# Optimization experiments

Measured on AMD Instinct MI355X. Metric: run time of the kernel, lower is better.

The kernel has to match this reference:

```python
import jax, jax.numpy as jnp
import numpy as np

H = 4  # attention heads


def _lstm(x, Wih, Whh, b, reverse=False):
    # x: [N, L, din] -> hidden sequence [N, L, dh]; PyTorch gate order i,f,g,o
    if reverse:
        x = x[:, ::-1, :]
    xT = jnp.swapaxes(x, 0, 1)  # [L, N, din]
    dh = Whh.shape[1]
    N = x.shape[0]

    def step(carry, xt):
        h, c = carry
        z = xt @ Wih.T + h @ Whh.T + b
        i, f, g, o = jnp.split(z, 4, axis=-1)
        c = jax.nn.sigmoid(f) * c + jax.nn.sigmoid(i) * jnp.tanh(g)
        h = jax.nn.sigmoid(o) * jnp.tanh(c)
        return (h, c), h

    h0 = jnp.zeros((N, dh), x.dtype)
    _, hs = jax.lax.scan(step, (h0, h0), xT)
    hs = jnp.swapaxes(hs, 0, 1)
    if reverse:
        hs = hs[:, ::-1, :]
    return hs


def setup_inputs() -> dict:
    key = jax.random.key(0)
    ks = jax.random.split(key, 24)
    B, T, D = 8, 128, 512
    C, L, U, V, E = 1000, 8, 16, 5000, 256

    def w(k, shape, fan_in):
        return jax.random.normal(k, shape, jnp.float32) * (1.0 / np.sqrt(fan_in))

    inp = {
        'model_embed': jax.random.normal(ks[0], (B, T, D), jnp.float32),
        'emb_table': w(ks[1], (V, E), E),
        'ctx_Wih_f': w(ks[2], (4 * E, E), E),
        'ctx_Whh_f': w(ks[3], (4 * E, E), E),
        'ctx_b_f': jnp.zeros((4 * E,), jnp.float32),
        'ctx_Wih_b': w(ks[4], (4 * E, E), E),
        'ctx_Whh_b': w(ks[5], (4 * E, E), E),
        'ctx_b_b': jnp.zeros((4 * E,), jnp.float32),
        'ctx_out_W': w(ks[6], (D, 2 * E), 2 * E),
        'hist_Wih': w(ks[7], (4 * D, D), D),
        'hist_Whh': w(ks[8], (4 * D, D), D),
        'hist_b': jnp.zeros((4 * D,), jnp.float32),
        'hist_out_W': w(ks[9], (D, D), D),
        'Wq': w(ks[10], (D, D), D),
        'Wk': w(ks[11], (D, D), D),
        'Wv': w(ks[12], (D, D), D),
        'Wo': w(ks[13], (D, D), D),
        'acoustic_W': w(ks[14], (D, D), D),
        'context_idxs': jax.random.randint(ks[15], (C, L), 0, V),
        'context_history_idx': jax.random.randint(ks[16], (B, U), 0, C),
        'context_ilens': jax.random.randint(ks[17], (C,), 1, L + 1),
        'context_history_ilens': jax.random.randint(ks[18], (B,), 1, U + 1),
    }
    return inp


def reference(model_embed, emb_table, ctx_Wih_f, ctx_Whh_f, ctx_b_f,
              ctx_Wih_b, ctx_Whh_b, ctx_b_b, ctx_out_W,
              hist_Wih, hist_Whh, hist_b, hist_out_W,
              Wq, Wk, Wv, Wo, acoustic_W,
              context_idxs, context_history_idx, context_ilens,
              context_history_ilens):
    C, L = context_idxs.shape
    B, T, D = model_embed.shape
    U = context_history_idx.shape[1]

    # --- ContextEncoderBiLSTM: embed -> BiLSTM -> proj -> length-masked mean ---
    emb = emb_table[context_idxs]                               # [C, L, E]
    hf = _lstm(emb, ctx_Wih_f, ctx_Whh_f, ctx_b_f)
    hb = _lstm(emb, ctx_Wih_b, ctx_Whh_b, ctx_b_b, reverse=True)
    seq = jnp.concatenate([hf, hb], -1) @ ctx_out_W.T           # [C, L, D]
    m = (jnp.arange(L)[None, :] < context_ilens[:, None]).astype(seq.dtype)
    ctx_mean = (seq * m[..., None]).sum(1) / context_ilens[:, None].astype(seq.dtype)  # [C, D]

    # --- history gather + ContextHistoryEncoderLSTM ---
    hist_in = ctx_mean[context_history_idx.reshape(-1)].reshape(B, U, D)
    hist = _lstm(hist_in, hist_Wih, hist_Whh, hist_b) @ hist_out_W.T  # [B, U, D]

    # --- fuse acoustic + history, attention-based adapter ---
    mp = model_embed @ acoustic_W.T                             # [B, T, D]
    fused = (mp[:, :, None, :] + hist[:, None, :, :]).reshape(B, T * U, D)
    dh = D // H
    q = (fused @ Wq.T).reshape(B, T * U, H, dh)
    k = (ctx_mean @ Wk.T).reshape(C, H, dh)
    v = (ctx_mean @ Wv.T).reshape(C, H, dh)
    scores = jnp.einsum('bqhd,chd->bhqc', q, k) / jnp.sqrt(jnp.asarray(dh, q.dtype))
    attn = jax.nn.softmax(scores, axis=-1)                      # [B, H, TU, C]
    out = (jnp.einsum('bhqc,chd->bqhd', attn, v).reshape(B, T * U, D) @ Wo.T)
    out = out.reshape(B, T, U, D)
    prob = attn.reshape(B, H, T, U, C).mean(1)                  # [B, T, U, C]
    logit = scores.reshape(B, H, T, U, C).mean(1)

    # --- batch greedy monotonic decoding (scan over T, full length) ---
    probT = jnp.moveaxis(prob, 1, 0)                            # [T, B, U, C]
    outT = jnp.moveaxis(out, 1, 0)                              # [T, B, U, D]
    b_idx = jnp.arange(B)

    def step(u, inp):
        p_t, o_t = inp
        u_c = jnp.minimum(u, U - 1)
        valid_u = jnp.minimum(u + 1, U - 1)
        tok = context_history_idx[b_idx, valid_u]
        blank_p = p_t[b_idx, u_c, 0]
        tok_p = p_t[b_idx, u_c, tok]
        upd = (tok_p > blank_p).astype(jnp.int32)
        return u_c + upd, (u_c, o_t[b_idx, u_c])

    u0 = jnp.zeros((B,), jnp.int32)
    _, (idx, o) = jax.lax.scan(step, u0, (probT, outT))
    o = jnp.moveaxis(o, 0, 1)                                   # [B, T, D]
    return o, logit, prob
```

## Files before the change

kernel.cpp:

```cpp
#include <hip/hip_runtime.h>
#include <math.h>

namespace {
constexpr int B_ = 8, T_ = 128, D_ = 512, C_ = 1000, L_ = 8, U_ = 16, E_ = 256, H_ = 4;
constexpr int VOC_ = 5000;
constexpr int DH_ = D_ / H_;
constexpr int E4_ = 4 * E_;
constexpr int D4_ = 4 * D_;
constexpr int TU_ = T_ * U_;
constexpr int HC_ = H_ * C_;
constexpr float SCALE_ = 0.088388347648318447f;

constexpr size_t XZ_    = 0;
constexpr size_t SM_    = 0;
constexpr size_t SH_    = SM_ + (size_t)B_ * T_ * HC_;
constexpr size_t AOUT_  = SH_ + (size_t)B_ * U_ * HC_;
constexpr size_t PVP_   = AOUT_ + (size_t)B_ * T_ * D_;
constexpr size_t REG_A  = 2ul * VOC_ * E4_;
constexpr size_t HPING  = REG_A;
constexpr size_t CST    = HPING + 2ul * C_ * E_;
constexpr size_t HPONG  = CST + 2ul * C_ * E_;
constexpr size_t HFALL  = HPONG + 2ul * C_ * E_;
constexpr size_t HBALL  = HFALL + (size_t)C_ * L_ * E_;
constexpr size_t CATM   = HBALL + (size_t)C_ * L_ * E_;
constexpr size_t CTXM   = CATM + (size_t)C_ * 2 * E_;
constexpr size_t KWS    = CTXM + (size_t)C_ * D_;
constexpr size_t VWS    = KWS + (size_t)C_ * D_;
constexpr size_t WQA    = VWS + (size_t)C_ * D_;
constexpr size_t WQH    = WQA + (size_t)D_ * D_;
constexpr size_t HXP    = WQH + (size_t)D_ * D_;
constexpr size_t HALL   = HXP + (size_t)B_ * U_ * D4_;
constexpr size_t HGLOB  = HALL + (size_t)B_ * U_ * D_;
constexpr size_t HG2    = HGLOB + (size_t)B_ * D_;
constexpr size_t HISTC  = HG2 + (size_t)B_ * D_;
constexpr size_t QM_    = HISTC + (size_t)B_ * D_;
constexpr size_t QH_    = QM_ + (size_t)B_ * T_ * D_;
constexpr size_t SMSUM  = QH_ + (size_t)B_ * U_ * D_;
constexpr size_t SHSUM  = SMSUM + (size_t)B_ * T_ * C_;
constexpr size_t DEN_   = SHSUM + (size_t)B_ * U_ * C_;
constexpr size_t BITS_  = DEN_ + (size_t)B_ * T_ * U_ * H_;
constexpr size_t USEL_  = BITS_ + 4096;
constexpr size_t WS_NEED = USEL_ + (size_t)B_ * T_;
}

__device__ __forceinline__ float fsig(float x)  { return 1.f / (1.f + __expf(-x)); }
__device__ __forceinline__ float ftanh(float x) { return 1.f - 2.f / (__expf(2.f * x) + 1.f); }
__device__ __forceinline__ void fma4(float4& a, float w, const float4& v) {
  a.x += w * v.x; a.y += w * v.y; a.z += w * v.z; a.w += w * v.w;
}

struct GemmP {
  const float* A1; int lda1;
  const int* ridx; int ridx_stride; int ridx_off;
  const float* W1; int ldw1;
  const float* bias;
  float* out; int ldc;
  int M, N, K;
  float scale;
  int a_zoff, w_zoff, c_zoff;
};

template <int TN>
__device__ __forceinline__ void gemm_core(const GemmP& g, int z) {
  constexpr int UN = TN / 16;
  constexpr int WP = TN / 64;
  __shared__ float As[16][68];
  __shared__ float Ws[16][TN + 4];
  const int m0 = blockIdx.y * 64;
  const int n0 = blockIdx.x * TN;
  if (m0 >= g.M || n0 >= g.N) return;
  const float* A1 = g.A1 + (long)z * g.a_zoff;
  const float* W1 = g.W1 + (long)z * g.w_zoff;
  float* out = g.out + (long)z * g.c_zoff;
  const int tid = threadIdx.x;
  const int tx = tid & 15, ty = tid >> 4;
  const int sr = tid >> 2, skq = (tid & 3) * 4;
  float acc[4][UN] = {};
  int sarow = -1;
  {
    const int gm = m0 + sr;
    if (gm < g.M) sarow = g.ridx ? g.ridx[gm * g.ridx_stride + g.ridx_off] : gm;
  }
  float4 pa, pw[WP];
  {
    pa = make_float4(0.f, 0.f, 0.f, 0.f);
    if (sarow >= 0) pa = *(const float4*)&A1[(long)sarow * g.lda1 + skq];
#pragma unroll
    for (int p = 0; p < WP; ++p) {
      const int gn = n0 + sr + p * 64;
      pw[p] = make_float4(0.f, 0.f, 0.f, 0.f);
      if (gn < g.N) pw[p] = *(const float4*)&W1[(long)gn * g.ldw1 + skq];
    }
  }
  for (int k0 = 0; k0 < g.K; k0 += 16) {
    As[skq][sr] = pa.x; As[skq + 1][sr] = pa.y; As[skq + 2][sr] = pa.z; As[skq + 3][sr] = pa.w;
#pragma unroll
    for (int p = 0; p < WP; ++p) {
      const int r = sr + p * 64;
      Ws[skq][r] = pw[p].x; Ws[skq + 1][r] = pw[p].y; Ws[skq + 2][r] = pw[p].z; Ws[skq + 3][r] = pw[p].w;
    }
    __syncthreads();
    const int kn = k0 + 16;
    if (kn < g.K) {
      pa = make_float4(0.f, 0.f, 0.f, 0.f);
      if (sarow >= 0) pa = *(const float4*)&A1[(long)sarow * g.lda1 + kn + skq];
#pragma unroll
      for (int p = 0; p < WP; ++p) {
        const int gn = n0 + sr + p * 64;
        pw[p] = make_float4(0.f, 0.f, 0.f, 0.f);
        if (gn < g.N) pw[p] = *(const float4*)&W1[(long)gn * g.ldw1 + kn + skq];
      }
    }
#pragma unroll
    for (int k = 0; k < 16; ++k) {
      const float4 a = *(const float4*)&As[k][ty * 4];
#pragma unroll
      for (int q = 0; q < UN / 4; ++q) {
        const float4 w = *(const float4*)&Ws[k][q * 64 + tx * 4];
        acc[0][q*4+0] += a.x * w.x; acc[0][q*4+1] += a.x * w.y; acc[0][q*4+2] += a.x * w.z; acc[0][q*4+3] += a.x * w.w;
        acc[1][q*4+0] += a.y * w.x; acc[1][q*4+1] += a.y * w.y; acc[1][q*4+2] += a.y * w.z; acc[1][q*4+3] += a.y * w.w;
        acc[2][q*4+0] += a.z * w.x; acc[2][q*4+1] += a.z * w.y; acc[2][q*4+2] += a.z * w.z; acc[2][q*4+3] += a.z * w.w;
        acc[3][q*4+0] += a.w * w.x; acc[3][q*4+1] += a.w * w.y; acc[3][q*4+2] += a.w * w.z; acc[3][q*4+3] += a.w * w.w;
      }
    }
    __syncthreads();
  }
#pragma unroll
  for (int i = 0; i < 4; ++i) {
    const int gm = m0 + ty * 4 + i;
    if (gm >= g.M) continue;
#pragma unroll
    for (int q = 0; q < UN / 4; ++q) {
#pragma unroll
      for (int j = 0; j < 4; ++j) {
        const int gn = n0 + q * 64 + tx * 4 + j;
        if (gn >= g.N) continue;
        float v2 = acc[i][q*4+j];
        if (g.bias) v2 += g.bias[gn];
        out[(long)gm * g.ldc + gn] = v2 * g.scale;
      }
    }
  }
}

__global__ __launch_bounds__(256) void k_gemm64(GemmP p)  { gemm_core<64>(p, blockIdx.z); }
__global__ __launch_bounds__(256) void k_gemm64x2(GemmP p0, GemmP p1, int zs) {
  int z = blockIdx.z;
  if (z < zs) gemm_core<64>(p0, z); else gemm_core<64>(p1, z - zs);
}
__global__ __launch_bounds__(256) void k_gemm64x3(GemmP p0, GemmP p1, GemmP p2) {
  int z = blockIdx.z;
  if (z == 0) gemm_core<64>(p0, 0);
  else if (z == 1) gemm_core<64>(p1, 0);
  else gemm_core<64>(p2, 0);
}

struct GemmB {
  const float* A; int lda;
  const float* W; int ldw;
  const float* bias;
  float* out; int ldc;
  int M, N, K;
  float scale;
  int a_zoff, w_zoff, c_zoff;
};

__device__ __forceinline__ void gemm_big_core(const GemmB& g, int z) {
  __shared__ float As[16][132];
  __shared__ float Ws[16][132];
  const int m0 = blockIdx.y * 128;
  const int n0 = blockIdx.x * 128;
  if (m0 >= g.M || n0 >= g.N) return;
  const float* A = g.A + (long)z * g.a_zoff;
  const float* W = g.W + (long)z * g.w_zoff;
  float* out = g.out + (long)z * g.c_zoff;
  const int tid = threadIdx.x;
  const int tx = tid & 15, ty = tid >> 4;
  const int sr = tid >> 2, skq = (tid & 3) * 4;
  float4 acc[2][2][4];
#pragma unroll
  for (int a = 0; a < 2; ++a)
#pragma unroll
    for (int b2 = 0; b2 < 2; ++b2)
#pragma unroll
      for (int i = 0; i < 4; ++i) acc[a][b2][i] = make_float4(0.f, 0.f, 0.f, 0.f);
  for (int k0 = 0; k0 < g.K; k0 += 16) {
#pragma unroll
    for (int p = 0; p < 2; ++p) {
      const int r = sr + p * 64;
      const int gm = m0 + r;
      float4 v = make_float4(0.f, 0.f, 0.f, 0.f);
      if (gm < g.M) v = *(const float4*)&A[(long)gm * g.lda + k0 + skq];
      As[skq][r] = v.x; As[skq + 1][r] = v.y; As[skq + 2][r] = v.z; As[skq + 3][r] = v.w;
      const int gn = n0 + r;
      float4 w = make_float4(0.f, 0.f, 0.f, 0.f);
      if (gn < g.N) w = *(const float4*)&W[(long)gn * g.ldw + k0 + skq];
      Ws[skq][r] = w.x; Ws[skq + 1][r] = w.y; Ws[skq + 2][r] = w.z; Ws[skq + 3][r] = w.w;
    }
    __syncthreads();
#pragma unroll
    for (int k = 0; k < 16; ++k) {
      const float4 a0 = *(const float4*)&As[k][ty * 4];
      const float4 a1 = *(const float4*)&As[k][64 + ty * 4];
      const float4 w0 = *(const float4*)&Ws[k][tx * 4];
      const float4 w1 = *(const float4*)&Ws[k][64 + tx * 4];
      fma4(acc[0][0][0], a0.x, w0); fma4(acc[0][0][1], a0.y, w0); fma4(acc[0][0][2], a0.z, w0); fma4(acc[0][0][3], a0.w, w0);
      fma4(acc[0][1][0], a0.x, w1); fma4(acc[0][1][1], a0.y, w1); fma4(acc[0][1][2], a0.z, w1); fma4(acc[0][1][3], a0.w, w1);
      fma4(acc[1][0][0], a1.x, w0); fma4(acc[1][0][1], a1.y, w0); fma4(acc[1][0][2], a1.z, w0); fma4(acc[1][0][3], a1.w, w0);
      fma4(acc[1][1][0], a1.x, w1); fma4(acc[1][1][1], a1.y, w1); fma4(acc[1][1][2], a1.z, w1); fma4(acc[1][1][3], a1.w, w1);
    }
    __syncthreads();
  }
#pragma unroll
  for (int a = 0; a < 2; ++a) {
#pragma unroll
    for (int i = 0; i < 4; ++i) {
      const int gm = m0 + a * 64 + ty * 4 + i;
      if (gm >= g.M) continue;
#pragma unroll
      for (int b2 = 0; b2 < 2; ++b2) {
        const int gn = n0 + b2 * 64 + tx * 4;
        if (gn >= g.N) continue;
        float4 v = acc[a][b2][i];
        if (g.bias) {
          v.x += g.bias[gn]; v.y += g.bias[gn + 1]; v.z += g.bias[gn + 2]; v.w += g.bias[gn + 3];
        }
        v.x *= g.scale; v.y *= g.scale; v.z *= g.scale; v.w *= g.scale;
        if (gn + 3 < g.N) {
          *(float4*)&out[(long)gm * g.ldc + gn] = v;
        } else {
          float vv[4] = {v.x, v.y, v.z, v.w};
          for (int j = 0; j < 4; ++j) if (gn + j < g.N) out[(long)gm * g.ldc + gn + j] = vv[j];
        }
      }
    }
  }
}

__global__ __launch_bounds__(256) void k_gemm_bigx2(GemmB p0, GemmB p1, int zs) {
  int z = blockIdx.z;
  if (z < zs) gemm_big_core(p0, z); else gemm_big_core(p1, z - zs);
}

__global__ __launch_bounds__(256) void k_gemm_nn(
    const float* __restrict__ A0, const float* __restrict__ B0, float* __restrict__ O0,
    const float* __restrict__ A1, const float* __restrict__ B1, float* __restrict__ O1) {
  const float* A = blockIdx.z ? A1 : A0;
  const float* B = blockIdx.z ? B1 : B0;
  float* O = blockIdx.z ? O1 : O0;
  __shared__ float As[16][68];
  __shared__ float Bs[16][68];
  const int m0 = blockIdx.y * 64, n0 = blockIdx.x * 64;
  const int tid = threadIdx.x;
  const int tx = tid & 15, ty = tid >> 4;
  const int sr = tid >> 2, skq = (tid & 3) * 4;
  float acc[4][4] = {};
  for (int k0 = 0; k0 < 512; k0 += 16) {
    {
      float4 v = *(const float4*)&A[(long)(m0 + sr) * 512 + k0 + skq];
      As[skq][sr] = v.x; As[skq + 1][sr] = v.y; As[skq + 2][sr] = v.z; As[skq + 3][sr] = v.w;
    }
#pragma unroll
    for (int p = 0; p < 4; ++p) {
      int idx = tid + p * 256;
      int kk = idx >> 6, jj = idx & 63;
      Bs[kk][jj] = B[(long)(k0 + kk) * 512 + n0 + jj];
    }
    __syncthreads();
#pragma unroll
    for (int k = 0; k < 16; ++k) {
      const float4 a = *(const float4*)&As[k][ty * 4];
      const float4 w = *(const float4*)&Bs[k][tx * 4];
      acc[0][0] += a.x * w.x; acc[0][1] += a.x * w.y; acc[0][2] += a.x * w.z; acc[0][3] += a.x * w.w;
      acc[1][0] += a.y * w.x; acc[1][1] += a.y * w.y; acc[1][2] += a.y * w.z; acc[1][3] += a.y * w.w;
      acc[2][0] += a.z * w.x; acc[2][1] += a.z * w.y; acc[2][2] += a.z * w.z; acc[2][3] += a.z * w.w;
      acc[3][0] += a.w * w.x; acc[3][1] += a.w * w.y; acc[3][2] += a.w * w.z; acc[3][3] += a.w * w.w;
    }
    __syncthreads();
  }
#pragma unroll
  for (int i = 0; i < 4; ++i)
#pragma unroll
    for (int j = 0; j < 4; ++j)
      O[(long)(m0 + ty * 4 + i) * 512 + n0 + tx * 4 + j] = acc[i][j];
}

__global__ __launch_bounds__(256) void k_ctx_step(
    const float* __restrict__ xz, const int* __restrict__ ctx_idxs,
    const float* __restrict__ Whh_f, const float* __restrict__ Whh_b,
    const float* __restrict__ h_prev, float* __restrict__ h_next,
    float* __restrict__ c_st,
    float* __restrict__ hf_all, float* __restrict__ hb_all, int t) {
  __shared__ float Hs[32][36];
  __shared__ float Wg[4][32][68];
  const int e0 = blockIdx.x * 64;
  const int c0 = blockIdx.y * 32;
  const int dir = blockIdx.z;
  const int tid = threadIdx.x;
  const float* Whh = dir ? Whh_b : Whh_f;
  const float* hp = h_prev + (size_t)dir * C_ * E_;
  const int cy = tid >> 4, ex = tid & 15;
  const int hcr = tid & 31, hkq = (tid >> 5) * 4;
  const int hc = c0 + hcr;
  float acc[4][2][4] = {};
  float4 phv, pwv[8];
  {
    phv = make_float4(0.f, 0.f, 0.f, 0.f);
    if (hc < C_) phv = *(const float4*)&hp[(size_t)hc * E_ + hkq];
#pragma unroll
    for (int p = 0; p < 8; ++p) {
      int idx = tid + p * 256;
      int ee = idx & 63, kq = ((idx >> 6) & 7) * 4, gg = idx >> 9;
      pwv[p] = *(const float4*)&Whh[(size_t)(gg * E_ + e0 + ee) * E_ + kq];
    }
  }
  for (int k0 = 0; k0 < E_; k0 += 32) {
    Hs[hkq][hcr] = phv.x; Hs[hkq + 1][hcr] = phv.y; Hs[hkq + 2][hcr] = phv.z; Hs[hkq + 3][hcr] = phv.w;
#pragma unroll
    for (int p = 0; p < 8; ++p) {
      int idx = tid + p * 256;
      int ee = idx & 63, kq = ((idx >> 6) & 7) * 4, gg = idx >> 9;
      Wg[gg][kq][ee] = pwv[p].x; Wg[gg][kq + 1][ee] = pwv[p].y; Wg[gg][kq + 2][ee] = pwv[p].z; Wg[gg][kq + 3][ee] = pwv[p].w;
    }
    __syncthreads();
    const int kn = k0 + 32;
    if (kn < E_) {
      phv = make_float4(0.f, 0.f, 0.f, 0.f);
      if (hc < C_) phv = *(const float4*)&hp[(size_t)hc * E_ + kn + hkq];
#pragma unroll
      for (int p = 0; p < 8; ++p) {
        int idx = tid + p * 256;
        int ee = idx & 63, kq = ((idx >> 6) & 7) * 4, gg = idx >> 9;
        pwv[p] = *(const float4*)&Whh[(size_t)(gg * E_ + e0 + ee) * E_ + kn + kq];
      }
    }
#pragma unroll
    for (int kk = 0; kk < 32; ++kk) {
      const float a0 = Hs[kk][cy * 2];
      const float a1 = Hs[kk][cy * 2 + 1];
#pragma unroll
      for (int gg = 0; gg < 4; ++gg) {
        const float4 w = *(const float4*)&Wg[gg][kk][ex * 4];
        acc[gg][0][0] += a0 * w.x; acc[gg][0][1] += a0 * w.y; acc[gg][0][2] += a0 * w.z; acc[gg][0][3] += a0 * w.w;
        acc[gg][1][0] += a1 * w.x; acc[gg][1][1] += a1 * w.y; acc[gg][1][2] += a1 * w.z; acc[gg][1][3] += a1 * w.w;
      }
    }
    __syncthreads();
  }
  const int lpos = dir ? (L_ - 1 - t) : t;
  const float* xz_dir = xz + (size_t)dir * VOC_ * E4_;
  float* c_state = c_st + (size_t)dir * C_ * E_;
  float* hn_out = h_next + (size_t)dir * C_ * E_;
  float* hall = dir ? hb_all : hf_all;
#pragma unroll
  for (int i = 0; i < 2; ++i) {
    const int c = c0 + cy * 2 + i;
    if (c >= C_) continue;
    const int e = e0 + ex * 4;
    const int tok = ctx_idxs[c * L_ + lpos];
    const float* xr = xz_dir + (size_t)tok * E4_;
    float zi[4], zf[4], zg[4], zo[4], cp[4], cn[4], hn[4];
    *(float4*)zi = *(const float4*)&xr[e];
    *(float4*)zf = *(const float4*)&xr[E_ + e];
    *(float4*)zg = *(const float4*)&xr[2 * E_ + e];
    *(float4*)zo = *(const float4*)&xr[3 * E_ + e];
    *(float4*)cp = *(const float4*)&c_state[(size_t)c * E_ + e];
#pragma unroll
    for (int j = 0; j < 4; ++j) {
      float vi = zi[j] + acc[0][i][j];
      float vf = zf[j] + acc[1][i][j];
      float vg = zg[j] + acc[2][i][j];
      float vo = zo[j] + acc[3][i][j];
      cn[j] = fsig(vf) * cp[j] + fsig(vi) * ftanh(vg);
      hn[j] = fsig(vo) * ftanh(cn[j]);
    }
    *(float4*)&c_state[(size_t)c * E_ + e] = *(float4*)cn;
    *(float4*)&hn_out[(size_t)c * E_ + e] = *(float4*)hn;
    *(float4*)&hall[((size_t)c * L_ + lpos) * E_ + e] = *(float4*)hn;
  }
}

__global__ __launch_bounds__(256) void k_ctx_mean(
    const float* __restrict__ hf_all, const float* __restrict__ hb_all,
    const int* __restrict__ ilens, float* __restrict__ cat_mean) {
  int idx = blockIdx.x * 256 + threadIdx.x;
  if (idx >= C_ * 2 * E_) return;
  int c = idx / (2 * E_), e = idx - c * 2 * E_;
  const float* src = (e < E_) ? hf_all : hb_all;
  int ee = e & (E_ - 1);
  int il = ilens[c];
  float s = 0.f;
#pragma unroll
  for (int l = 0; l < L_; ++l)
    if (l < il) s += src[((size_t)c * L_ + l) * E_ + ee];
  cat_mean[idx] = s / (float)il;
}

__global__ __launch_bounds__(256) void k_hist_step2(
    const float* __restrict__ xproj, const float* __restrict__ Whh,
    const float* __restrict__ hprev, float* __restrict__ hcur,
    float* __restrict__ cstG, float* __restrict__ hall, int u) {
  __shared__ float Wl[32][516];
  __shared__ float hb[8][520];
  const int tid = threadIdx.x;
  const int e0 = blockIdx.x * 8;
  {
    int lr = tid >> 3, part = tid & 7;
    int g2 = lr >> 3, e2 = lr & 7;
    const float* src = Whh + (size_t)(g2 * D_ + e0 + e2) * D_;
#pragma unroll
    for (int i = 0; i < 16; ++i) {
      int k4 = part + i * 8;
      *(float4*)&Wl[lr][k4 * 4] = *(const float4*)&src[k4 * 4];
    }
  }
  {
    int b2 = tid >> 5, part = tid & 31;
#pragma unroll
    for (int i = 0; i < 4; ++i) {
      int k4 = part + i * 32;
      float4 v = make_float4(0.f, 0.f, 0.f, 0.f);
      if (u > 0) v = *(const float4*)&hprev[(size_t)b2 * D_ + k4 * 4];
      *(float4*)&hb[b2][k4 * 4] = v;
    }
  }
  __syncthreads();
  const int b = tid >> 5, g = (tid >> 3) & 3, e = tid & 7;
  const int lr = tid & 31;
  float dot = 0.f;
#pragma unroll 8
  for (int k4 = 0; k4 < 128; ++k4) {
    float4 w = *(const float4*)&Wl[lr][k4 * 4];
    float4 h4 = *(const float4*)&hb[b][k4 * 4];
    dot += w.x * h4.x + w.y * h4.y + w.z * h4.z + w.w * h4.w;
  }
  float z = dot + xproj[((size_t)b * U_ + u) * D4_ + g * D_ + e0 + e];
  const int l = tid & 63;
  const int base = (l & 32) | e;
  float zi = __shfl(z, base, 64);
  float zf = __shfl(z, base + 8, 64);
  float zg = __shfl(z, base + 16, 64);
  float zo = __shfl(z, base + 24, 64);
  if (g == 0) {
    float cp = (u > 0) ? cstG[(size_t)b * D_ + e0 + e] : 0.f;
    float cn = fsig(zf) * cp + fsig(zi) * ftanh(zg);
    cstG[(size_t)b * D_ + e0 + e] = cn;
    float hv = fsig(zo) * ftanh(cn);
    hcur[(size_t)b * D_ + e0 + e] = hv;
    hall[((size_t)b * U_ + u) * D_ + e0 + e] = hv;
  }
}

__global__ __launch_bounds__(256) void k_rowexp(
    float* __restrict__ Sm, float* __restrict__ Sh,
    float* __restrict__ SmS, float* __restrict__ ShS) {
  int row = blockIdx.x;
  float* base; float* sumo;
  if (row < B_ * T_) { base = Sm + (size_t)row * HC_; sumo = SmS + (size_t)row * C_; }
  else { int r2 = row - B_ * T_; base = Sh + (size_t)r2 * HC_; sumo = ShS + (size_t)r2 * C_; }
  int tid = threadIdx.x;
  for (int c = tid; c < C_; c += 256) {
    float s = base[c] + base[C_ + c] + base[2 * C_ + c] + base[3 * C_ + c];
    sumo[c] = 0.25f * s;
  }
  __syncthreads();
  int h = tid >> 6, lane = tid & 63;
  float* p = base + (size_t)h * C_;
  float mx = -1e30f;
  for (int c = lane; c < C_; c += 64) mx = fmaxf(mx, p[c]);
#pragma unroll
  for (int o = 32; o; o >>= 1) mx = fmaxf(mx, __shfl_xor(mx, o));
  for (int c = lane; c < C_; c += 64) p[c] = __expf(p[c] - mx);
}

__global__ __launch_bounds__(256) void k_den(
    const float* __restrict__ EM, const float* __restrict__ EH,
    float* __restrict__ den) {
  const int bt = blockIdx.x;
  const int b = bt >> 7;
  const int h = threadIdx.x >> 6, lane = threadIdx.x & 63;
  const float* emp = EM + ((size_t)bt * H_ + h) * C_;
  float em[16];
#pragma unroll
  for (int i = 0; i < 16; ++i) {
    int c = lane + i * 64;
    em[i] = (c < C_) ? emp[c] : 0.f;
  }
  for (int u = 0; u < U_; ++u) {
    const float* ehp = EH + (((size_t)b * U_ + u) * H_ + h) * C_;
    float s = 0.f;
#pragma unroll
    for (int i = 0; i < 16; ++i) {
      int c = lane + i * 64;
      if (c < C_) s += em[i] * ehp[c];
    }
#pragma unroll
    for (int o = 32; o; o >>= 1) s += __shfl_xor(s, o);
    if (lane == 0) den[((size_t)bt * U_ + u) * H_ + h] = s;
  }
}

__global__ __launch_bounds__(256) void k_plw(
    const float* __restrict__ EM, const float* __restrict__ EH,
    const float* __restrict__ SmS, const float* __restrict__ ShS,
    const float* __restrict__ den, const int* __restrict__ hidx,
    float* __restrict__ prob, float* __restrict__ logit,
    unsigned char* __restrict__ bits) {
  __shared__ float sEM[H_][1008];
  __shared__ float sSS[1000];
  __shared__ float sB[4], sT[4];
  const int bt = blockIdx.x >> 2;
  const int ug = blockIdx.x & 3;
  const int b = bt >> 7;
  const int tid = threadIdx.x;
  for (int i = tid; i < H_ * C_; i += 256) sEM[i / C_][i % C_] = EM[(size_t)bt * HC_ + i];
  for (int c = tid; c < C_; c += 256) sSS[c] = SmS[(size_t)bt * C_ + c];
  __syncthreads();
#pragma unroll
  for (int j = 0; j < 4; ++j) {
    const int u = ug * 4 + j;
    const int valid = (u + 1 < U_ - 1) ? (u + 1) : (U_ - 1);
    const int tok = hidx[b * U_ + valid];
    const float* dnp = den + ((size_t)bt * U_ + u) * H_;
    const float i0 = 0.25f / dnp[0], i1 = 0.25f / dnp[1];
    const float i2 = 0.25f / dnp[2], i3 = 0.25f / dnp[3];
    const float* eh0 = EH + ((size_t)b * U_ + u) * HC_;
    const float* shs = ShS + ((size_t)b * U_ + u) * C_;
    size_t obase = ((size_t)bt * U_ + u) * C_;
    for (int c = tid; c < C_; c += 256) {
      float pr = sEM[0][c] * eh0[c] * i0 + sEM[1][c] * eh0[C_ + c] * i1
               + sEM[2][c] * eh0[2 * C_ + c] * i2 + sEM[3][c] * eh0[3 * C_ + c] * i3;
      __builtin_nontemporal_store(pr, &prob[obase + c]);
      __builtin_nontemporal_store(sSS[c] + shs[c], &logit[obase + c]);
      if (c == 0) sB[j] = pr;
      if (c == tok) sT[j] = pr;
    }
  }
  __syncthreads();
  if (tid < 4) bits[bt * U_ + ug * 4 + tid] = (sT[tid] > sB[tid]) ? 1 : 0;
}

__global__ __launch_bounds__(64) void k_scan(
    const unsigned char* __restrict__ bits, int* __restrict__ u_sel) {
  __shared__ unsigned char sb[B_ * T_ * U_];
  int tid = threadIdx.x;
  for (int i = tid; i < B_ * T_ * U_; i += 64) sb[i] = bits[i];
  __syncthreads();
  if (tid < B_) {
    int u = 0;
    for (int t = 0; t < T_; ++t) {
      int uc = (u < U_ - 1) ? u : (U_ - 1);
      u_sel[tid * T_ + t] = uc;
      u = uc + (int)sb[(tid * T_ + t) * U_ + uc];
    }
  }
}

__global__ __launch_bounds__(256) void k_pvg2(
    const float* __restrict__ EM, const float* __restrict__ EH,
    const float* __restrict__ den, const int* __restrict__ u_sel,
    const float* __restrict__ vmat, float* __restrict__ pvp) {
  constexpr int KC = 64;
  __shared__ float wS[2][4][4][KC + 4];
  __shared__ float invS[8][4];
  __shared__ int bS[8], tS[8], uS[8];
  const int tid = threadIdx.x;
  const int cblk = blockIdx.y;
  if (tid < 32) {
    int g8 = tid >> 2, hh = tid & 3;
    int bt = blockIdx.x * 8 + g8;
    int b = bt >> 7, t = bt & 127;
    int u = u_sel[bt];
    if (hh == 0) { bS[g8] = b; tS[g8] = t; uS[g8] = u; }
    invS[g8][hh] = 1.f / den[((size_t)bt * U_ + u) * H_ + hh];
  }
  __syncthreads();
  const int sub = tid >> 7, lt = tid & 127;
  const int d = lt * 4;
  const int h = lt >> 5;
  float4 acc[4];
  acc[0] = acc[1] = acc[2] = acc[3] = make_float4(0.f, 0.f, 0.f, 0.f);
  const int cbeg = cblk * 128;
  const int cend = (cbeg + 128 < C_) ? (cbeg + 128) : C_;
  for (int c0 = cbeg; c0 < cend; c0 += KC) {
#pragma unroll
    for (int p = 0; p < 8; ++p) {
      int idx = tid + p * 256;
      int cc = idx & 63;
      int rest = idx >> 6;
      int hh = rest & 3, gg = (rest >> 2) & 3, ss = rest >> 4;
      int g8 = ss * 4 + gg;
      int c = c0 + cc;
      float w = 0.f;
      if (c < C_) {
        int b = bS[g8], t = tS[g8], u = uS[g8];
        float em = EM[(((size_t)b * T_ + t) * H_ + hh) * C_ + c];
        float eh = EH[(((size_t)b * U_ + u) * H_ + hh) * C_ + c];
        w = em * eh * invS[g8][hh];
      }
      wS[ss][gg][hh][cc] = w;
    }
    __syncthreads();
#pragma unroll 4
    for (int q = 0; q < KC / 4; ++q) {
      const float4 w0 = *(const float4*)&wS[sub][0][h][q * 4];
      const float4 w1 = *(const float4*)&wS[sub][1][h][q * 4];
      const float4 w2 = *(const float4*)&wS[sub][2][h][q * 4];
      const float4 w3 = *(const float4*)&wS[sub][3][h][q * 4];
      int c = c0 + q * 4;
      float4 v;
      if (c < C_) { v = *(const float4*)&vmat[(size_t)c * D_ + d];
        fma4(acc[0], w0.x, v); fma4(acc[1], w1.x, v); fma4(acc[2], w2.x, v); fma4(acc[3], w3.x, v); }
      if (c + 1 < C_) { v = *(const float4*)&vmat[(size_t)(c + 1) * D_ + d];
        fma4(acc[0], w0.y, v); fma4(acc[1], w1.y, v); fma4(acc[2], w2.y, v); fma4(acc[3], w3.y, v); }
      if (c + 2 < C_) { v = *(const float4*)&vmat[(size_t)(c + 2) * D_ + d];
        fma4(acc[0], w0.z, v); fma4(acc[1], w1.z, v); fma4(acc[2], w2.z, v); fma4(acc[3], w3.z, v); }
      if (c + 3 < C_) { v = *(const float4*)&vmat[(size_t)(c + 3) * D_ + d];
        fma4(acc[0], w0.w, v); fma4(acc[1], w1.w, v); fma4(acc[2], w2.w, v); fma4(acc[3], w3.w, v); }
    }
    __syncthreads();
  }
  float* pout = pvp + (size_t)cblk * (B_ * T_) * D_;
#pragma unroll
  for (int g = 0; g < 4; ++g) {
    int bt = (bS[sub * 4 + g] << 7) + tS[sub * 4 + g];
    *(float4*)&pout[(size_t)bt * D_ + d] = acc[g];
  }
}

__global__ __launch_bounds__(256) void k_pvred(
    const float* __restrict__ pvp, float* __restrict__ aout) {
  const size_t i = ((size_t)blockIdx.x * 256 + threadIdx.x) * 4;
  float4 s = *(const float4*)&pvp[i];
#pragma unroll
  for (int k = 1; k < 8; ++k) {
    const float4 v = *(const float4*)&pvp[(size_t)k * (B_ * T_) * D_ + i];
    s.x += v.x; s.y += v.y; s.z += v.z; s.w += v.w;
  }
  *(float4*)&aout[i] = s;
}

extern "C" void kernel_launch(void* const* d_in, const int* in_sizes, int n_in,
                              void* d_out, int out_size, void* d_ws, size_t ws_size,
                              hipStream_t stream) {
  const float* model_embed = (const float*)d_in[0];
  const float* emb_table   = (const float*)d_in[1];
  const float* Wih_f = (const float*)d_in[2];
  const float* Whh_f = (const float*)d_in[3];
  const float* b_f   = (const float*)d_in[4];
  const float* Wih_b = (const float*)d_in[5];
  const float* Whh_b = (const float*)d_in[6];
  const float* b_b   = (const float*)d_in[7];
  const float* ctx_out_W  = (const float*)d_in[8];
  const float* hist_Wih   = (const float*)d_in[9];
  const float* hist_Whh   = (const float*)d_in[10];
  const float* hist_b     = (const float*)d_in[11];
  const float* hist_out_W = (const float*)d_in[12];
  const float* Wq = (const float*)d_in[13];
  const float* Wk = (const float*)d_in[14];
  const float* Wv = (const float*)d_in[15];
  const float* Wo = (const float*)d_in[16];
  const float* acoustic_W = (const float*)d_in[17];
  const int* ctx_idxs = (const int*)d_in[18];
  const int* hidx     = (const int*)d_in[19];
  const int* ilens    = (const int*)d_in[20];

  if (ws_size < WS_NEED * sizeof(float)) return;

  float* ws = (float*)d_ws;
  float* o_out     = (float*)d_out;
  float* logit_out = o_out + (size_t)B_ * T_ * D_;
  float* prob_out  = logit_out + (size_t)B_ * T_ * U_ * C_;

  hipMemsetAsync(ws + HPING, 0, 4ul * C_ * E_ * sizeof(float), stream);

  k_gemm_nn<<<dim3(8, 8, 2), 256, 0, stream>>>(
      Wq, acoustic_W, ws + WQA, Wq, hist_out_W, ws + WQH);

  {
    GemmB pf{};
    pf.A = emb_table; pf.lda = E_;
    pf.W = Wih_f; pf.ldw = E_;
    pf.bias = b_f;
    pf.out = ws + XZ_; pf.ldc = E4_;
    pf.M = VOC_; pf.N = E4_; pf.K = E_; pf.scale = 1.f;
    GemmB pb = pf;
    pb.W = Wih_b; pb.bias = b_b; pb.out = ws + XZ_ + (size_t)VOC_ * E4_;
    k_gemm_bigx2<<<dim3(8, (VOC_ + 127) / 128, 2), 256, 0, stream>>>(pf, pb, 1);
  }

  for (int t = 0; t < L_; ++t) {
    float* hp = ws + ((t & 1) ? HPONG : HPING);
    float* hn = ws + ((t & 1) ? HPING : HPONG);
    k_ctx_step<<<dim3(4, 32, 2), 256, 0, stream>>>(
        ws + XZ_, ctx_idxs, Whh_f, Whh_b, hp, hn, ws + CST,
        ws + HFALL, ws + HBALL, t);
  }

  k_ctx_mean<<<dim3((C_ * 2 * E_ + 255) / 256), 256, 0, stream>>>(
      ws + HFALL, ws + HBALL, ilens, ws + CATM);
  {
    GemmP p{};
    p.A1 = ws + CATM; p.lda1 = 2 * E_;
    p.W1 = ctx_out_W; p.ldw1 = 2 * E_;
    p.out = ws + CTXM; p.ldc = D_; p.M = C_; p.N = D_; p.K = 2 * E_; p.scale = 1.f;
    k_gemm64<<<dim3(8, 16, 1), 256, 0, stream>>>(p);
  }

  {
    GemmP pk{};
    pk.A1 = ws + CTXM; pk.lda1 = D_;
    pk.W1 = Wk; pk.ldw1 = D_;
    pk.out = ws + KWS; pk.ldc = D_; pk.M = C_; pk.N = D_; pk.K = D_; pk.scale = SCALE_;
    GemmP pv = pk;
    pv.W1 = Wv; pv.out = ws + VWS; pv.scale = 1.f;
    GemmP ph{};
    ph.A1 = ws + CTXM; ph.lda1 = D_;
    ph.ridx = hidx; ph.ridx_stride = 1; ph.ridx_off = 0;
    ph.W1 = hist_Wih; ph.ldw1 = D_;
    ph.bias = hist_b;
    ph.out = ws + HXP; ph.ldc = D4_; ph.M = B_ * U_; ph.N = D4_; ph.K = D_; ph.scale = 1.f;
    k_gemm64x3<<<dim3(32, 16, 3), 256, 0, stream>>>(pk, pv, ph);
  }

  for (int u = 0; u < U_; ++u) {
    const float* hp = ws + ((u & 1) ? HG2 : HGLOB);
    float* hc = ws + ((u & 1) ? HGLOB : HG2);
    k_hist_step2<<<dim3(64), 256, 0, stream>>>(
        ws + HXP, hist_Whh, hp, hc, ws + HISTC, ws + HALL, u);
  }

  {
    GemmP pm{};
    pm.A1 = model_embed; pm.lda1 = D_;
    pm.W1 = ws + WQA; pm.ldw1 = D_;
    pm.out = ws + QM_; pm.ldc = D_; pm.M = B_ * T_; pm.N = D_; pm.K = D_; pm.scale = 1.f;
    GemmP ph = pm;
    ph.A1 = ws + HALL; ph.W1 = ws + WQH; ph.out = ws + QH_; ph.M = B_ * U_;
    k_gemm64x2<<<dim3(8, 16, 2), 256, 0, stream>>>(pm, ph, 1);
  }

  {
    GemmB pm{};
    pm.A = ws + QM_; pm.lda = D_;
    pm.W = ws + KWS; pm.ldw = D_;
    pm.out = ws + SM_; pm.ldc = HC_; pm.M = B_ * T_; pm.N = C_; pm.K = DH_; pm.scale = 1.f;
    pm.a_zoff = DH_; pm.w_zoff = DH_; pm.c_zoff = C_;
    GemmB ph = pm;
    ph.A = ws + QH_; ph.out = ws + SH_; ph.M = B_ * U_;
    k_gemm_bigx2<<<dim3(8, 8, 8), 256, 0, stream>>>(pm, ph, 4);
  }

  k_rowexp<<<dim3(B_ * T_ + B_ * U_), 256, 0, stream>>>(
      ws + SM_, ws + SH_, ws + SMSUM, ws + SHSUM);

  k_den<<<dim3(B_ * T_), 256, 0, stream>>>(ws + SM_, ws + SH_, ws + DEN_);

  k_plw<<<dim3(B_ * T_ * 4), 256, 0, stream>>>(
      ws + SM_, ws + SH_, ws + SMSUM, ws + SHSUM, ws + DEN_, hidx,
      prob_out, logit_out, (unsigned char*)(ws + BITS_));

  k_scan<<<dim3(1), 64, 0, stream>>>((const unsigned char*)(ws + BITS_), (int*)(ws + USEL_));

  k_pvg2<<<dim3(128, 8), 256, 0, stream>>>(
      ws + SM_, ws + SH_, ws + DEN_, (const int*)(ws + USEL_), ws + VWS, ws + PVP_);
  k_pvred<<<dim3((B_ * T_ * D_) / (256 * 4)), 256, 0, stream>>>(ws + PVP_, ws + AOUT_);

  {
    GemmP p{};
    p.A1 = ws + AOUT_; p.lda1 = D_;
    p.W1 = Wo; p.ldw1 = D_;
    p.out = o_out; p.ldc = D_; p.M = B_ * T_; p.N = D_; p.K = D_; p.scale = 1.f;
    k_gemm64<<<dim3(8, 16, 1), 256, 0, stream>>>(p);
  }
}
```

Before: 786.1 us.

## Split LSTM step gates across thread groups and drop big-tile GEMM

The context LSTM step kernel now handles 16 rows per block instead of 32, with the two 128-thread halves each computing two of the four gate blocks and exchanging partial results through a shared-memory buffer before the cell update. This doubles the grid size to give more blocks per step on the large GPU and cuts per-thread accumulator registers. The 128x128 GEMM path is removed and its callers (embedding projection and score GEMMs) are moved to the existing 64-tile GEMM with larger grids. The trade is more blocks and more redundant weight loads in exchange for higher occupancy and parallelism.

```diff
diff --git a/kernel.cpp b/kernel.cpp
--- a/kernel.cpp
+++ b/kernel.cpp
@@ -155,93 +155,6 @@
   else gemm_core<64>(p2, 0);
 }
 
-struct GemmB {
-  const float* A; int lda;
-  const float* W; int ldw;
-  const float* bias;
-  float* out; int ldc;
-  int M, N, K;
-  float scale;
-  int a_zoff, w_zoff, c_zoff;
-};
-
-__device__ __forceinline__ void gemm_big_core(const GemmB& g, int z) {
-  __shared__ float As[16][132];
-  __shared__ float Ws[16][132];
-  const int m0 = blockIdx.y * 128;
-  const int n0 = blockIdx.x * 128;
-  if (m0 >= g.M || n0 >= g.N) return;
-  const float* A = g.A + (long)z * g.a_zoff;
-  const float* W = g.W + (long)z * g.w_zoff;
-  float* out = g.out + (long)z * g.c_zoff;
-  const int tid = threadIdx.x;
-  const int tx = tid & 15, ty = tid >> 4;
-  const int sr = tid >> 2, skq = (tid & 3) * 4;
-  float4 acc[2][2][4];
-#pragma unroll
-  for (int a = 0; a < 2; ++a)
-#pragma unroll
-    for (int b2 = 0; b2 < 2; ++b2)
-#pragma unroll
-      for (int i = 0; i < 4; ++i) acc[a][b2][i] = make_float4(0.f, 0.f, 0.f, 0.f);
-  for (int k0 = 0; k0 < g.K; k0 += 16) {
-#pragma unroll
-    for (int p = 0; p < 2; ++p) {
-      const int r = sr + p * 64;
-      const int gm = m0 + r;
-      float4 v = make_float4(0.f, 0.f, 0.f, 0.f);
-      if (gm < g.M) v = *(const float4*)&A[(long)gm * g.lda + k0 + skq];
-      As[skq][r] = v.x; As[skq + 1][r] = v.y; As[skq + 2][r] = v.z; As[skq + 3][r] = v.w;
-      const int gn = n0 + r;
-      float4 w = make_float4(0.f, 0.f, 0.f, 0.f);
-      if (gn < g.N) w = *(const float4*)&W[(long)gn * g.ldw + k0 + skq];
-      Ws[skq][r] = w.x; Ws[skq + 1][r] = w.y; Ws[skq + 2][r] = w.z; Ws[skq + 3][r] = w.w;
-    }
-    __syncthreads();
-#pragma unroll
-    for (int k = 0; k < 16; ++k) {
-      const float4 a0 = *(const float4*)&As[k][ty * 4];
-      const float4 a1 = *(const float4*)&As[k][64 + ty * 4];
-      const float4 w0 = *(const float4*)&Ws[k][tx * 4];
-      const float4 w1 = *(const float4*)&Ws[k][64 + tx * 4];
-      fma4(acc[0][0][0], a0.x, w0); fma4(acc[0][0][1], a0.y, w0); fma4(acc[0][0][2], a0.z, w0); fma4(acc[0][0][3], a0.w, w0);
-      fma4(acc[0][1][0], a0.x, w1); fma4(acc[0][1][1], a0.y, w1); fma4(acc[0][1][2], a0.z, w1); fma4(acc[0][1][3], a0.w, w1);
-      fma4(acc[1][0][0], a1.x, w0); fma4(acc[1][0][1], a1.y, w0); fma4(acc[1][0][2], a1.z, w0); fma4(acc[1][0][3], a1.w, w0);
-      fma4(acc[1][1][0], a1.x, w1); fma4(acc[1][1][1], a1.y, w1); fma4(acc[1][1][2], a1.z, w1); fma4(acc[1][1][3], a1.w, w1);
-    }
-    __syncthreads();
-  }
-#pragma unroll
-  for (int a = 0; a < 2; ++a) {
-#pragma unroll
-    for (int i = 0; i < 4; ++i) {
-      const int gm = m0 + a * 64 + ty * 4 + i;
-      if (gm >= g.M) continue;
-#pragma unroll
-      for (int b2 = 0; b2 < 2; ++b2) {
-        const int gn = n0 + b2 * 64 + tx * 4;
-        if (gn >= g.N) continue;
-        float4 v = acc[a][b2][i];
-        if (g.bias) {
-          v.x += g.bias[gn]; v.y += g.bias[gn + 1]; v.z += g.bias[gn + 2]; v.w += g.bias[gn + 3];
-        }
-        v.x *= g.scale; v.y *= g.scale; v.z *= g.scale; v.w *= g.scale;
-        if (gn + 3 < g.N) {
-          *(float4*)&out[(long)gm * g.ldc + gn] = v;
-        } else {
-          float vv[4] = {v.x, v.y, v.z, v.w};
-          for (int j = 0; j < 4; ++j) if (gn + j < g.N) out[(long)gm * g.ldc + gn + j] = vv[j];
-        }
-      }
-    }
-  }
-}
-
-__global__ __launch_bounds__(256) void k_gemm_bigx2(GemmB p0, GemmB p1, int zs) {
-  int z = blockIdx.z;
-  if (z < zs) gemm_big_core(p0, z); else gemm_big_core(p1, z - zs);
-}
-
 __global__ __launch_bounds__(256) void k_gemm_nn(
     const float* __restrict__ A0, const float* __restrict__ B0, float* __restrict__ O0,
     const float* __restrict__ A1, const float* __restrict__ B1, float* __restrict__ O1) {
@@ -291,31 +204,37 @@
     const float* __restrict__ h_prev, float* __restrict__ h_next,
     float* __restrict__ c_st,
     float* __restrict__ hf_all, float* __restrict__ hb_all, int t) {
-  __shared__ float Hs[32][36];
+  __shared__ float Hs[32][20];
   __shared__ float Wg[4][32][68];
+  __shared__ float zb[4][16][68];
   const int e0 = blockIdx.x * 64;
-  const int c0 = blockIdx.y * 32;
+  const int c0 = blockIdx.y * 16;
   const int dir = blockIdx.z;
   const int tid = threadIdx.x;
   const float* Whh = dir ? Whh_b : Whh_f;
   const float* hp = h_prev + (size_t)dir * C_ * E_;
-  const int cy = tid >> 4, ex = tid & 15;
-  const int hcr = tid & 31, hkq = (tid >> 5) * 4;
+  const int gp = tid >> 7;
+  const int rem = tid & 127;
+  const int cy = rem >> 4;
+  const int ex = rem & 15;
+  const bool hstage = (tid < 128);
+  const int hcr = tid & 15, hkq = ((tid >> 4) & 7) * 4;
   const int hc = c0 + hcr;
-  float acc[4][2][4] = {};
-  float4 phv, pwv[8];
-  {
-    phv = make_float4(0.f, 0.f, 0.f, 0.f);
-    if (hc < C_) phv = *(const float4*)&hp[(size_t)hc * E_ + hkq];
-#pragma unroll
-    for (int p = 0; p < 8; ++p) {
-      int idx = tid + p * 256;
-      int ee = idx & 63, kq = ((idx >> 6) & 7) * 4, gg = idx >> 9;
-      pwv[p] = *(const float4*)&Whh[(size_t)(gg * E_ + e0 + ee) * E_ + kq];
-    }
+  float4 acc4[2][2];
+  acc4[0][0] = acc4[0][1] = acc4[1][0] = acc4[1][1] = make_float4(0.f, 0.f, 0.f, 0.f);
+  float4 phv = make_float4(0.f, 0.f, 0.f, 0.f);
+  float4 pwv[8];
+  if (hstage && hc < C_) phv = *(const float4*)&hp[(size_t)hc * E_ + hkq];
+#pragma unroll
+  for (int p = 0; p < 8; ++p) {
+    int idx = tid + p * 256;
+    int ee = idx & 63, kq = ((idx >> 6) & 7) * 4, gg = idx >> 9;
+    pwv[p] = *(const float4*)&Whh[(size_t)(gg * E_ + e0 + ee) * E_ + kq];
   }
   for (int k0 = 0; k0 < E_; k0 += 32) {
-    Hs[hkq][hcr] = phv.x; Hs[hkq + 1][hcr] = phv.y; Hs[hkq + 2][hcr] = phv.z; Hs[hkq + 3][hcr] = phv.w;
+    if (hstage) {
+      Hs[hkq][hcr] = phv.x; Hs[hkq + 1][hcr] = phv.y; Hs[hkq + 2][hcr] = phv.z; Hs[hkq + 3][hcr] = phv.w;
+    }
 #pragma unroll
     for (int p = 0; p < 8; ++p) {
       int idx = tid + p * 256;
@@ -326,7 +245,7 @@
     const int kn = k0 + 32;
     if (kn < E_) {
       phv = make_float4(0.f, 0.f, 0.f, 0.f);
-      if (hc < C_) phv = *(const float4*)&hp[(size_t)hc * E_ + kn + hkq];
+      if (hstage && hc < C_) phv = *(const float4*)&hp[(size_t)hc * E_ + kn + hkq];
 #pragma unroll
       for (int p = 0; p < 8; ++p) {
         int idx = tid + p * 256;
@@ -339,24 +258,29 @@
       const float a0 = Hs[kk][cy * 2];
       const float a1 = Hs[kk][cy * 2 + 1];
 #pragma unroll
-      for (int gg = 0; gg < 4; ++gg) {
-        const float4 w = *(const float4*)&Wg[gg][kk][ex * 4];
-        acc[gg][0][0] += a0 * w.x; acc[gg][0][1] += a0 * w.y; acc[gg][0][2] += a0 * w.z; acc[gg][0][3] += a0 * w.w;
-        acc[gg][1][0] += a1 * w.x; acc[gg][1][1] += a1 * w.y; acc[gg][1][2] += a1 * w.z; acc[gg][1][3] += a1 * w.w;
+      for (int gg = 0; gg < 2; ++gg) {
+        const float4 w = *(const float4*)&Wg[gp * 2 + gg][kk][ex * 4];
+        fma4(acc4[gg][0], a0, w);
+        fma4(acc4[gg][1], a1, w);
       }
     }
     __syncthreads();
   }
+#pragma unroll
+  for (int gg = 0; gg < 2; ++gg) {
+    *(float4*)&zb[gp * 2 + gg][cy * 2 + 0][ex * 4] = acc4[gg][0];
+    *(float4*)&zb[gp * 2 + gg][cy * 2 + 1][ex * 4] = acc4[gg][1];
+  }
+  __syncthreads();
   const int lpos = dir ? (L_ - 1 - t) : t;
   const float* xz_dir = xz + (size_t)dir * VOC_ * E4_;
   float* c_state = c_st + (size_t)dir * C_ * E_;
   float* hn_out = h_next + (size_t)dir * C_ * E_;
   float* hall = dir ? hb_all : hf_all;
-#pragma unroll
-  for (int i = 0; i < 2; ++i) {
-    const int c = c0 + cy * 2 + i;
-    if (c >= C_) continue;
-    const int e = e0 + ex * 4;
+  const int oc = tid >> 4, oe = (tid & 15) * 4;
+  const int c = c0 + oc;
+  if (c < C_) {
+    const int e = e0 + oe;
     const int tok = ctx_idxs[c * L_ + lpos];
     const float* xr = xz_dir + (size_t)tok * E4_;
     float zi[4], zf[4], zg[4], zo[4], cp[4], cn[4], hn[4];
@@ -367,10 +291,10 @@
     *(float4*)cp = *(const float4*)&c_state[(size_t)c * E_ + e];
 #pragma unroll
     for (int j = 0; j < 4; ++j) {
-      float vi = zi[j] + acc[0][i][j];
-      float vf = zf[j] + acc[1][i][j];
-      float vg = zg[j] + acc[2][i][j];
-      float vo = zo[j] + acc[3][i][j];
+      float vi = zi[j] + zb[0][oc][oe + j];
+      float vf = zf[j] + zb[1][oc][oe + j];
+      float vg = zg[j] + zb[2][oc][oe + j];
+      float vo = zo[j] + zb[3][oc][oe + j];
       cn[j] = fsig(vf) * cp[j] + fsig(vi) * ftanh(vg);
       hn[j] = fsig(vo) * ftanh(cn[j]);
     }
@@ -678,21 +602,21 @@
       Wq, acoustic_W, ws + WQA, Wq, hist_out_W, ws + WQH);
 
   {
-    GemmB pf{};
-    pf.A = emb_table; pf.lda = E_;
-    pf.W = Wih_f; pf.ldw = E_;
+    GemmP pf{};
+    pf.A1 = emb_table; pf.lda1 = E_;
+    pf.W1 = Wih_f; pf.ldw1 = E_;
     pf.bias = b_f;
     pf.out = ws + XZ_; pf.ldc = E4_;
     pf.M = VOC_; pf.N = E4_; pf.K = E_; pf.scale = 1.f;
-    GemmB pb = pf;
-    pb.W = Wih_b; pb.bias = b_b; pb.out = ws + XZ_ + (size_t)VOC_ * E4_;
-    k_gemm_bigx2<<<dim3(8, (VOC_ + 127) / 128, 2), 256, 0, stream>>>(pf, pb, 1);
+    GemmP pb = pf;
+    pb.W1 = Wih_b; pb.bias = b_b; pb.out = ws + XZ_ + (size_t)VOC_ * E4_;
+    k_gemm64x2<<<dim3(E4_ / 64, (VOC_ + 63) / 64, 2), 256, 0, stream>>>(pf, pb, 1);
   }
 
   for (int t = 0; t < L_; ++t) {
     float* hp = ws + ((t & 1) ? HPONG : HPING);
     float* hn = ws + ((t & 1) ? HPING : HPONG);
-    k_ctx_step<<<dim3(4, 32, 2), 256, 0, stream>>>(
+    k_ctx_step<<<dim3(4, (C_ + 15) / 16, 2), 256, 0, stream>>>(
         ws + XZ_, ctx_idxs, Whh_f, Whh_b, hp, hn, ws + CST,
         ws + HFALL, ws + HBALL, t);
   }
@@ -741,14 +665,14 @@
   }
 
   {
-    GemmB pm{};
-    pm.A = ws + QM_; pm.lda = D_;
-    pm.W = ws + KWS; pm.ldw = D_;
+    GemmP pm{};
+    pm.A1 = ws + QM_; pm.lda1 = D_;
+    pm.W1 = ws + KWS; pm.ldw1 = D_;
     pm.out = ws + SM_; pm.ldc = HC_; pm.M = B_ * T_; pm.N = C_; pm.K = DH_; pm.scale = 1.f;
     pm.a_zoff = DH_; pm.w_zoff = DH_; pm.c_zoff = C_;
-    GemmB ph = pm;
-    ph.A = ws + QH_; ph.out = ws + SH_; ph.M = B_ * U_;
-    k_gemm_bigx2<<<dim3(8, 8, 8), 256, 0, stream>>>(pm, ph, 4);
+    GemmP ph = pm;
+    ph.A1 = ws + QH_; ph.out = ws + SH_; ph.M = B_ * U_;
+    k_gemm64x2<<<dim3(16, 16, 8), 256, 0, stream>>>(pm, ph, 4);
   }
 
   k_rowexp<<<dim3(B_ * T_ + B_ * U_), 256, 0, stream>>>(
```

Measured after the change: 782.9 us. Within noise of the previous version (-0.4%).
